# Kernel optimization log

Measured on AMD Instinct MI355X. Metric: run time of the kernel, lower is better.

Reference implementation:

```python
import jax, jax.numpy as jnp
import numpy as np

HEIGHT = 10
IN_DIM = 256
OUT_DIM = 16
BATCH = 65536


def _and_weight(height):
    # Fixed +/-1 tree-structured routing matrix [leaf_nodes, int_nodes]
    int_nodes = 2 ** height - 1
    leaf = 2 ** height
    w = np.zeros((leaf, int_nodes), dtype=np.float32)
    for i in range(height):
        num = 2 ** i
        start = num - 1
        for j in range(start, start + num):
            rb = leaf // num * (j - start)
            rm = rb + leaf // (2 * num)
            re = rb + leaf // num
            w[rb:rm, j] = 1.0
            w[rm:re, j] = -1.0
    return jnp.asarray(w)


def setup_inputs() -> dict:
    key = jax.random.key(0)
    k0, k1, k2, k3 = jax.random.split(key, 4)
    int_nodes = 2 ** HEIGHT - 1
    leaf = 2 ** HEIGHT
    return {
        "x": jax.random.normal(k0, (BATCH, IN_DIM), jnp.float32),
        "W_pred": jax.random.normal(k1, (int_nodes, IN_DIM), jnp.float32) / np.float32(np.sqrt(IN_DIM)),
        "b_pred": jnp.zeros((int_nodes,), jnp.float32),
        "W_or": jax.random.normal(k2, (OUT_DIM, leaf), jnp.float32) / np.float32(np.sqrt(leaf)),
        "action_stds": jax.random.normal(k3, (OUT_DIM, leaf), jnp.float32),
    }


def reference(x, W_pred, b_pred, W_or, action_stds):
    # predicate linear: [B, int_nodes]
    pred_z = x @ W_pred.T + b_pred
    # ScaleBinarizer1 (STE): scale = mean |z| per sample, binarize to {0, fac}
    fac = jax.lax.stop_gradient(jnp.mean(jnp.abs(pred_z), axis=-1, keepdims=True))
    hard = jnp.where(pred_z >= 0, fac, jnp.zeros_like(fac))
    pred_bin = pred_z + jax.lax.stop_gradient(hard - pred_z)  # straight-through
    pred_a = 2.0 * pred_bin - fac  # +/- fac (sign of pred_z scaled)
    # fixed tree AND layer: [B, leaf]
    W_and = _and_weight(HEIGHT)
    and_z = pred_a @ W_and.T
    and_a = jax.nn.softmax(and_z, axis=-1)
    # Sparser1 (STE): hard one-hot of the argmax leaf
    onehot = jax.nn.one_hot(jnp.argmax(and_a, axis=-1), and_a.shape[-1], dtype=and_a.dtype)
    and_a = and_a + jax.lax.stop_gradient(onehot - and_a)
    # OR layer + softmax over classes
    or_z = and_a @ W_or.T  # [B, out_dim]
    out = jax.nn.softmax(or_z, axis=-1)
    # per-action std: sum over leaves of and_a * action_stds, clamped
    std = jnp.clip(jnp.einsum("bl,ol->bo", and_a, action_stds), -20.0, 2.0)
    return out, std
```

## Files before the change

kernel.cpp:

```cpp
#include <hip/hip_runtime.h>
#include <stdint.h>


#define BATCH   65536
#define IN_DIM  256
#define NLEVEL  10
#define NLEAF   1024
#define OUT_DIM 16
#define EPS_TIE 0.02f
#define WB_U32  (1023 * 128)

#define DPP_QUAD_XOR1   0xB1
#define DPP_QUAD_XOR2   0x4E
#define DPP_HALF_MIRROR 0x141

template <int CTRL>
__device__ __forceinline__ float dpp_xfer(float v) {
    return __int_as_float(__builtin_amdgcn_update_dpp(
        0, __float_as_int(v), CTRL, 0xf, 0xf, true));
}
__device__ __forceinline__ float group8_sum(float v) {
    v += dpp_xfer<DPP_QUAD_XOR1>(v);
    v += dpp_xfer<DPP_QUAD_XOR2>(v);
    v += dpp_xfer<DPP_HALF_MIRROR>(v);
    return v;
}
__device__ __forceinline__ float group8_max(float v) {
    v = fmaxf(v, dpp_xfer<DPP_QUAD_XOR1>(v));
    v = fmaxf(v, dpp_xfer<DPP_QUAD_XOR2>(v));
    v = fmaxf(v, dpp_xfer<DPP_HALF_MIRROR>(v));
    return v;
}

__device__ __forceinline__ float blo(uint32_t u) { return __uint_as_float(u << 16); }
__device__ __forceinline__ float bhi(uint32_t u) { return __uint_as_float(u & 0xffff0000u); }

__global__ __launch_bounds__(256) void dgt_prep(
    const float* __restrict__ W, uint32_t* __restrict__ Wb)
{
    int i = blockIdx.x * 256 + threadIdx.x;
    if (i < WB_U32) {
        uint32_t ua = __float_as_uint(W[2 * i]);
        uint32_t ub = __float_as_uint(W[2 * i + 1]);
        uint32_t ra = (ua + 0x7fffu + ((ua >> 16) & 1u)) >> 16;
        uint32_t rb = (ub + 0x7fffu + ((ub >> 16) & 1u)) >> 16;
        Wb[i] = ra | (rb << 16);
    }
}

__device__ __forceinline__ int tree_sign_f64(
    float4 x0a, float4 x0b, float4 x1a, float4 x1b,
    float4 x2a, float4 x2b, float4 x3a, float4 x3b,
    const float* wrow, float bias, int l)
{
    double A0 = 0.0, A1 = 0.0, A2 = 0.0, A3 = 0.0;
#define ACC64(K, XA, XB)                                                     \
    {                                                                        \
        float4 wa = *reinterpret_cast<const float4*>(wrow + (K)*64 + l * 8); \
        float4 wb = *reinterpret_cast<const float4*>(wrow + (K)*64 + l * 8 + 4); \
        A0 += (double)XA.x * (double)wa.x; A1 += (double)XA.y * (double)wa.y; \
        A2 += (double)XA.z * (double)wa.z; A3 += (double)XA.w * (double)wa.w; \
        A0 += (double)XB.x * (double)wb.x; A1 += (double)XB.y * (double)wb.y; \
        A2 += (double)XB.z * (double)wb.z; A3 += (double)XB.w * (double)wb.w; \
    }
    ACC64(0, x0a, x0b) ACC64(1, x1a, x1b) ACC64(2, x2a, x2b) ACC64(3, x3a, x3b)
#undef ACC64
    double Z = (A0 + A1) + (A2 + A3);
    #pragma unroll
    for (int off = 4; off > 0; off >>= 1)
        Z += __shfl_xor(Z, off, 64);
    Z += (double)bias;
    return (Z < 0.0) ? 1 : 0;
}

__global__ __launch_bounds__(256, 2) void dgt_bf16(
    const float* __restrict__ x,
    const uint32_t* __restrict__ Wb,
    const float* __restrict__ W_pred,
    const float* __restrict__ b_pred,
    const float* __restrict__ W_or,
    const float* __restrict__ a_std,
    float* __restrict__ out)
{
    const int lane = threadIdx.x & 63;
    const int wid  = threadIdx.x >> 6;
    const int l    = lane & 7;
    const int g    = lane >> 3;
    const int sample = blockIdx.x * 32 + wid * 8 + g;

    const float* xrow = x + (size_t)sample * IN_DIM;
    float4 x0a = *reinterpret_cast<const float4*>(xrow +   0 + l * 8);
    float4 x0b = *reinterpret_cast<const float4*>(xrow +   4 + l * 8);
    float4 x1a = *reinterpret_cast<const float4*>(xrow +  64 + l * 8);
    float4 x1b = *reinterpret_cast<const float4*>(xrow +  68 + l * 8);
    float4 x2a = *reinterpret_cast<const float4*>(xrow + 128 + l * 8);
    float4 x2b = *reinterpret_cast<const float4*>(xrow + 132 + l * 8);
    float4 x3a = *reinterpret_cast<const float4*>(xrow + 192 + l * 8);
    float4 x3b = *reinterpret_cast<const float4*>(xrow + 196 + l * 8);

    int node = 0, pos = 0;
    float bcur = b_pred[0];

    #pragma unroll
    for (int lvl = 0; lvl < NLEVEL; ++lvl) {
        const uint32_t* wb = Wb + (size_t)node * 128;
        uint4 u0 = *reinterpret_cast<const uint4*>(wb +  0 + l * 4);
        uint4 u1 = *reinterpret_cast<const uint4*>(wb + 32 + l * 4);
        uint4 u2 = *reinterpret_cast<const uint4*>(wb + 64 + l * 4);
        uint4 u3 = *reinterpret_cast<const uint4*>(wb + 96 + l * 4);

        float bL = 0.f, bR = 0.f;
        if (lvl < NLEVEL - 1) {
            bL = b_pred[2 * node + 1];
            bR = b_pred[2 * node + 2];
        }

        float a0 = 0.f, a1 = 0.f, a2 = 0.f, a3 = 0.f;
#define ACCB(U, XA, XB)                                     \
        a0 += XA.x * blo(U.x); a1 += XA.y * bhi(U.x);       \
        a2 += XA.z * blo(U.y); a3 += XA.w * bhi(U.y);       \
        a0 += XB.x * blo(U.z); a1 += XB.y * bhi(U.z);       \
        a2 += XB.z * blo(U.w); a3 += XB.w * bhi(U.w);
        ACCB(u0, x0a, x0b)
        ACCB(u1, x1a, x1b)
        ACCB(u2, x2a, x2b)
        ACCB(u3, x3a, x3b)
#undef ACCB
        float z = group8_sum((a0 + a1) + (a2 + a3)) + bcur;

        int right;
        if (__builtin_expect(fabsf(z) >= EPS_TIE, 1))
            right = (z < 0.f) ? 1 : 0;
        else
            right = tree_sign_f64(x0a, x0b, x1a, x1b, x2a, x2b, x3a, x3b,
                                  W_pred + (size_t)node * IN_DIM, bcur, l);

        pos  = 2 * pos + right;
        node = 2 * node + 1 + right;
        if (lvl < NLEVEL - 1) bcur = right ? bR : bL;
    }
    const int leaf = pos;

    float zx = W_or[(size_t)(2 * l)     * NLEAF + leaf];
    float zy = W_or[(size_t)(2 * l + 1) * NLEAF + leaf];
    float m  = group8_max(fmaxf(zx, zy));
    float ex = __expf(zx - m), ey = __expf(zy - m);
    float s  = group8_sum(ex + ey);
    *reinterpret_cast<float2*>(out + (size_t)sample * OUT_DIM + 2 * l) =
        make_float2(ex / s, ey / s);

    float dx = a_std[(size_t)(2 * l)     * NLEAF + leaf];
    float dy = a_std[(size_t)(2 * l + 1) * NLEAF + leaf];
    *reinterpret_cast<float2*>(out + (size_t)BATCH * OUT_DIM
                               + (size_t)sample * OUT_DIM + 2 * l) =
        make_float2(fminf(fmaxf(dx, -20.f), 2.f),
                    fminf(fmaxf(dy, -20.f), 2.f));
}

__device__ __forceinline__ int tree_sign_f64_r8(
    float4 x0, float4 x1, float4 x2, float4 x3,
    float4 x4, float4 x5, float4 x6, float4 x7,
    const float* wrow, float bias, int l)
{
    double A0 = 0.0, A1 = 0.0, A2 = 0.0, A3 = 0.0;
#define ACC64(K, XV)                                                        \
    {                                                                       \
        float4 w = *reinterpret_cast<const float4*>(wrow + (K)*32 + l * 4); \
        A0 += (double)XV.x * (double)w.x; A1 += (double)XV.y * (double)w.y; \
        A2 += (double)XV.z * (double)w.z; A3 += (double)XV.w * (double)w.w; \
    }
    ACC64(0, x0) ACC64(1, x1) ACC64(2, x2) ACC64(3, x3)
    ACC64(4, x4) ACC64(5, x5) ACC64(6, x6) ACC64(7, x7)
#undef ACC64
    double Z = (A0 + A1) + (A2 + A3);
    #pragma unroll
    for (int off = 4; off > 0; off >>= 1)
        Z += __shfl_xor(Z, off, 64);
    Z += (double)bias;
    return (Z < 0.0) ? 1 : 0;
}

__global__ __launch_bounds__(256, 2) void dgt_f32(
    const float* __restrict__ x,
    const float* __restrict__ W_pred,
    const float* __restrict__ b_pred,
    const float* __restrict__ W_or,
    const float* __restrict__ a_std,
    float* __restrict__ out)
{
    const int lane = threadIdx.x & 63;
    const int wid  = threadIdx.x >> 6;
    const int l    = lane & 7;
    const int g    = lane >> 3;
    const int sample = blockIdx.x * 32 + wid * 8 + g;

    const float* xrow = x + (size_t)sample * IN_DIM;
    float4 x0 = *reinterpret_cast<const float4*>(xrow +   0 + l * 4);
    float4 x1 = *reinterpret_cast<const float4*>(xrow +  32 + l * 4);
    float4 x2 = *reinterpret_cast<const float4*>(xrow +  64 + l * 4);
    float4 x3 = *reinterpret_cast<const float4*>(xrow +  96 + l * 4);
    float4 x4 = *reinterpret_cast<const float4*>(xrow + 128 + l * 4);
    float4 x5 = *reinterpret_cast<const float4*>(xrow + 160 + l * 4);
    float4 x6 = *reinterpret_cast<const float4*>(xrow + 192 + l * 4);
    float4 x7 = *reinterpret_cast<const float4*>(xrow + 224 + l * 4);

    int node = 0, pos = 0;
    float bcur = b_pred[0];
    const float* wrow = W_pred;

    #pragma unroll
    for (int lvl = 0; lvl < NLEVEL; ++lvl) {
        float4 w0 = *reinterpret_cast<const float4*>(wrow +   0 + l * 4);
        float4 w1 = *reinterpret_cast<const float4*>(wrow +  32 + l * 4);
        float4 w2 = *reinterpret_cast<const float4*>(wrow +  64 + l * 4);
        float4 w3 = *reinterpret_cast<const float4*>(wrow +  96 + l * 4);
        float4 w4 = *reinterpret_cast<const float4*>(wrow + 128 + l * 4);
        float4 w5 = *reinterpret_cast<const float4*>(wrow + 160 + l * 4);
        float4 w6 = *reinterpret_cast<const float4*>(wrow + 192 + l * 4);
        float4 w7 = *reinterpret_cast<const float4*>(wrow + 224 + l * 4);

        float bL = 0.f, bR = 0.f;
        if (lvl < NLEVEL - 1) {
            bL = b_pred[2 * node + 1];
            bR = b_pred[2 * node + 2];
        }

        float a0, a1, a2, a3;
        a0  = x0.x * w0.x; a1  = x0.y * w0.y; a2  = x0.z * w0.z; a3  = x0.w * w0.w;
        a0 += x1.x * w1.x; a1 += x1.y * w1.y; a2 += x1.z * w1.z; a3 += x1.w * w1.w;
        a0 += x2.x * w2.x; a1 += x2.y * w2.y; a2 += x2.z * w2.z; a3 += x2.w * w2.w;
        a0 += x3.x * w3.x; a1 += x3.y * w3.y; a2 += x3.z * w3.z; a3 += x3.w * w3.w;
        a0 += x4.x * w4.x; a1 += x4.y * w4.y; a2 += x4.z * w4.z; a3 += x4.w * w4.w;
        a0 += x5.x * w5.x; a1 += x5.y * w5.y; a2 += x5.z * w5.z; a3 += x5.w * w5.w;
        a0 += x6.x * w6.x; a1 += x6.y * w6.y; a2 += x6.z * w6.z; a3 += x6.w * w6.w;
        a0 += x7.x * w7.x; a1 += x7.y * w7.y; a2 += x7.z * w7.z; a3 += x7.w * w7.w;
        float z = group8_sum((a0 + a1) + (a2 + a3)) + bcur;

        int right;
        if (__builtin_expect(fabsf(z) >= 1e-3f, 1))
            right = (z < 0.f) ? 1 : 0;
        else
            right = tree_sign_f64_r8(x0, x1, x2, x3, x4, x5, x6, x7,
                                     wrow, bcur, l);

        pos  = 2 * pos + right;
        node = 2 * node + 1 + right;
        if (lvl < NLEVEL - 1) {
            bcur = right ? bR : bL;
            wrow = W_pred + (size_t)node * IN_DIM;
        }
    }
    const int leaf = pos;

    float zx = W_or[(size_t)(2 * l)     * NLEAF + leaf];
    float zy = W_or[(size_t)(2 * l + 1) * NLEAF + leaf];
    float m  = group8_max(fmaxf(zx, zy));
    float ex = __expf(zx - m), ey = __expf(zy - m);
    float s  = group8_sum(ex + ey);
    *reinterpret_cast<float2*>(out + (size_t)sample * OUT_DIM + 2 * l) =
        make_float2(ex / s, ey / s);

    float dx = a_std[(size_t)(2 * l)     * NLEAF + leaf];
    float dy = a_std[(size_t)(2 * l + 1) * NLEAF + leaf];
    *reinterpret_cast<float2*>(out + (size_t)BATCH * OUT_DIM
                               + (size_t)sample * OUT_DIM + 2 * l) =
        make_float2(fminf(fmaxf(dx, -20.f), 2.f),
                    fminf(fmaxf(dy, -20.f), 2.f));
}

extern "C" void kernel_launch(void* const* d_in, const int* in_sizes, int n_in,
                              void* d_out, int out_size, void* d_ws, size_t ws_size,
                              hipStream_t stream) {
    const float* x      = (const float*)d_in[0];
    const float* W_pred = (const float*)d_in[1];
    const float* b_pred = (const float*)d_in[2];
    const float* W_or   = (const float*)d_in[3];
    const float* a_std  = (const float*)d_in[4];
    float* out = (float*)d_out;

    if (ws_size >= (size_t)WB_U32 * 4) {
        uint32_t* Wb = (uint32_t*)d_ws;
        hipLaunchKernelGGL(dgt_prep, dim3((WB_U32 + 255) / 256), dim3(256),
                           0, stream, W_pred, Wb);
        hipLaunchKernelGGL(dgt_bf16, dim3(BATCH / 32), dim3(256), 0, stream,
                           x, Wb, W_pred, b_pred, W_or, a_std, out);
    } else {
        hipLaunchKernelGGL(dgt_f32, dim3(BATCH / 32), dim3(256), 0, stream,
                           x, W_pred, b_pred, W_or, a_std, out);
    }
}
```

Baseline: 43.09 us.

## Stage top tree levels' bf16 weights in LDS, use fp32 global for last two levels

Each block of 512 threads copies the bf16-packed weights for the first 255 internal nodes (levels 0-7) into padded LDS and walks those levels from shared memory. The last two levels read full fp32 rows from global memory with a tighter tie threshold, so the bf16 conversion now covers only the staged rows. Blocks double in size to amortise the roughly 130 KB LDS fill. The fill is a large per-block cost, and the LDS footprint probably limits occupancy to one block per CU.

```diff
diff --git a/kernel.cpp b/kernel.cpp
--- a/kernel.cpp
+++ b/kernel.cpp
@@ -2,13 +2,14 @@
 #include <stdint.h>
 
 
-#define BATCH   65536
-#define IN_DIM  256
-#define NLEVEL  10
-#define NLEAF   1024
-#define OUT_DIM 16
-#define EPS_TIE 0.02f
-#define WB_U32  (1023 * 128)
+#define BATCH     65536
+#define IN_DIM    256
+#define NLEAF     1024
+#define OUT_DIM   16
+#define LDS_ROWS  255
+#define ROW_U32   128
+#define ROW_PAD   132
+#define STAGE_U32 (LDS_ROWS * ROW_U32)
 
 #define DPP_QUAD_XOR1   0xB1
 #define DPP_QUAD_XOR2   0x4E
@@ -39,7 +40,7 @@
     const float* __restrict__ W, uint32_t* __restrict__ Wb)
 {
     int i = blockIdx.x * 256 + threadIdx.x;
-    if (i < WB_U32) {
+    if (i < STAGE_U32) {
         uint32_t ua = __float_as_uint(W[2 * i]);
         uint32_t ub = __float_as_uint(W[2 * i + 1]);
         uint32_t ra = (ua + 0x7fffu + ((ua >> 16) & 1u)) >> 16;
@@ -73,7 +74,7 @@
     return (Z < 0.0) ? 1 : 0;
 }
 
-__global__ __launch_bounds__(256, 2) void dgt_bf16(
+__global__ __launch_bounds__(512, 2) void dgt_main(
     const float* __restrict__ x,
     const uint32_t* __restrict__ Wb,
     const float* __restrict__ W_pred,
@@ -82,11 +83,29 @@
     const float* __restrict__ a_std,
     float* __restrict__ out)
 {
+    __shared__ __align__(16) uint32_t sW[LDS_ROWS * ROW_PAD];
+
+    {
+        const uint4* src = reinterpret_cast<const uint4*>(Wb);
+        #pragma unroll
+        for (int s = 0; s < 16; ++s) {
+            int q = threadIdx.x + s * 512;
+            if (q < STAGE_U32 / 4) {
+                int j   = q * 4;
+                int row = j >> 7;
+                int col = j & 127;
+                uint4 v = src[q];
+                *reinterpret_cast<uint4*>(&sW[row * ROW_PAD + col]) = v;
+            }
+        }
+    }
+    __syncthreads();
+
     const int lane = threadIdx.x & 63;
     const int wid  = threadIdx.x >> 6;
     const int l    = lane & 7;
     const int g    = lane >> 3;
-    const int sample = blockIdx.x * 32 + wid * 8 + g;
+    const int sample = blockIdx.x * 64 + wid * 8 + g;
 
     const float* xrow = x + (size_t)sample * IN_DIM;
     float4 x0a = *reinterpret_cast<const float4*>(xrow +   0 + l * 8);
@@ -102,18 +121,15 @@
     float bcur = b_pred[0];
 
     #pragma unroll
-    for (int lvl = 0; lvl < NLEVEL; ++lvl) {
-        const uint32_t* wb = Wb + (size_t)node * 128;
-        uint4 u0 = *reinterpret_cast<const uint4*>(wb +  0 + l * 4);
-        uint4 u1 = *reinterpret_cast<const uint4*>(wb + 32 + l * 4);
-        uint4 u2 = *reinterpret_cast<const uint4*>(wb + 64 + l * 4);
-        uint4 u3 = *reinterpret_cast<const uint4*>(wb + 96 + l * 4);
-
-        float bL = 0.f, bR = 0.f;
-        if (lvl < NLEVEL - 1) {
-            bL = b_pred[2 * node + 1];
-            bR = b_pred[2 * node + 2];
-        }
+    for (int lvl = 0; lvl < 8; ++lvl) {
+        const uint32_t* wr = sW + node * ROW_PAD;
+        uint4 u0 = *reinterpret_cast<const uint4*>(wr +  0 + l * 4);
+        uint4 u1 = *reinterpret_cast<const uint4*>(wr + 32 + l * 4);
+        uint4 u2 = *reinterpret_cast<const uint4*>(wr + 64 + l * 4);
+        uint4 u3 = *reinterpret_cast<const uint4*>(wr + 96 + l * 4);
+
+        float bL = b_pred[2 * node + 1];
+        float bR = b_pred[2 * node + 2];
 
         float a0 = 0.f, a1 = 0.f, a2 = 0.f, a3 = 0.f;
 #define ACCB(U, XA, XB)                                     \
@@ -129,7 +145,7 @@
         float z = group8_sum((a0 + a1) + (a2 + a3)) + bcur;
 
         int right;
-        if (__builtin_expect(fabsf(z) >= EPS_TIE, 1))
+        if (__builtin_expect(fabsf(z) >= 0.02f, 1))
             right = (z < 0.f) ? 1 : 0;
         else
             right = tree_sign_f64(x0a, x0b, x1a, x1b, x2a, x2b, x3a, x3b,
@@ -137,7 +153,48 @@
 
         pos  = 2 * pos + right;
         node = 2 * node + 1 + right;
-        if (lvl < NLEVEL - 1) bcur = right ? bR : bL;
+        bcur = right ? bR : bL;
+    }
+
+    #pragma unroll
+    for (int lvl = 8; lvl < 10; ++lvl) {
+        const float* wrow = W_pred + (size_t)node * IN_DIM;
+        float4 w0a = *reinterpret_cast<const float4*>(wrow +   0 + l * 8);
+        float4 w0b = *reinterpret_cast<const float4*>(wrow +   4 + l * 8);
+        float4 w1a = *reinterpret_cast<const float4*>(wrow +  64 + l * 8);
+        float4 w1b = *reinterpret_cast<const float4*>(wrow +  68 + l * 8);
+        float4 w2a = *reinterpret_cast<const float4*>(wrow + 128 + l * 8);
+        float4 w2b = *reinterpret_cast<const float4*>(wrow + 132 + l * 8);
+        float4 w3a = *reinterpret_cast<const float4*>(wrow + 192 + l * 8);
+        float4 w3b = *reinterpret_cast<const float4*>(wrow + 196 + l * 8);
+
+        float bL = 0.f, bR = 0.f;
+        if (lvl < 9) {
+            bL = b_pred[2 * node + 1];
+            bR = b_pred[2 * node + 2];
+        }
+
+        float a0, a1, a2, a3;
+        a0  = x0a.x * w0a.x; a1  = x0a.y * w0a.y; a2  = x0a.z * w0a.z; a3  = x0a.w * w0a.w;
+        a0 += x0b.x * w0b.x; a1 += x0b.y * w0b.y; a2 += x0b.z * w0b.z; a3 += x0b.w * w0b.w;
+        a0 += x1a.x * w1a.x; a1 += x1a.y * w1a.y; a2 += x1a.z * w1a.z; a3 += x1a.w * w1a.w;
+        a0 += x1b.x * w1b.x; a1 += x1b.y * w1b.y; a2 += x1b.z * w1b.z; a3 += x1b.w * w1b.w;
+        a0 += x2a.x * w2a.x; a1 += x2a.y * w2a.y; a2 += x2a.z * w2a.z; a3 += x2a.w * w2a.w;
+        a0 += x2b.x * w2b.x; a1 += x2b.y * w2b.y; a2 += x2b.z * w2b.z; a3 += x2b.w * w2b.w;
+        a0 += x3a.x * w3a.x; a1 += x3a.y * w3a.y; a2 += x3a.z * w3a.z; a3 += x3a.w * w3a.w;
+        a0 += x3b.x * w3b.x; a1 += x3b.y * w3b.y; a2 += x3b.z * w3b.z; a3 += x3b.w * w3b.w;
+        float z = group8_sum((a0 + a1) + (a2 + a3)) + bcur;
+
+        int right;
+        if (__builtin_expect(fabsf(z) >= 1e-3f, 1))
+            right = (z < 0.f) ? 1 : 0;
+        else
+            right = tree_sign_f64(x0a, x0b, x1a, x1b, x2a, x2b, x3a, x3b,
+                                  wrow, bcur, l);
+
+        pos  = 2 * pos + right;
+        node = 2 * node + 1 + right;
+        if (lvl < 9) bcur = right ? bR : bL;
     }
     const int leaf = pos;
 
@@ -209,7 +266,7 @@
     const float* wrow = W_pred;
 
     #pragma unroll
-    for (int lvl = 0; lvl < NLEVEL; ++lvl) {
+    for (int lvl = 0; lvl < 10; ++lvl) {
         float4 w0 = *reinterpret_cast<const float4*>(wrow +   0 + l * 4);
         float4 w1 = *reinterpret_cast<const float4*>(wrow +  32 + l * 4);
         float4 w2 = *reinterpret_cast<const float4*>(wrow +  64 + l * 4);
@@ -220,7 +277,7 @@
         float4 w7 = *reinterpret_cast<const float4*>(wrow + 224 + l * 4);
 
         float bL = 0.f, bR = 0.f;
-        if (lvl < NLEVEL - 1) {
+        if (lvl < 9) {
             bL = b_pred[2 * node + 1];
             bR = b_pred[2 * node + 2];
         }
@@ -245,7 +302,7 @@
 
         pos  = 2 * pos + right;
         node = 2 * node + 1 + right;
-        if (lvl < NLEVEL - 1) {
+        if (lvl < 9) {
             bcur = right ? bR : bL;
             wrow = W_pred + (size_t)node * IN_DIM;
         }
@@ -278,11 +335,11 @@
     const float* a_std  = (const float*)d_in[4];
     float* out = (float*)d_out;
 
-    if (ws_size >= (size_t)WB_U32 * 4) {
+    if (ws_size >= (size_t)STAGE_U32 * 4) {
         uint32_t* Wb = (uint32_t*)d_ws;
-        hipLaunchKernelGGL(dgt_prep, dim3((WB_U32 + 255) / 256), dim3(256),
+        hipLaunchKernelGGL(dgt_prep, dim3((STAGE_U32 + 255) / 256), dim3(256),
                            0, stream, W_pred, Wb);
-        hipLaunchKernelGGL(dgt_bf16, dim3(BATCH / 32), dim3(256), 0, stream,
+        hipLaunchKernelGGL(dgt_main, dim3(BATCH / 64), dim3(512), 0, stream,
                            x, Wb, W_pred, b_pred, W_or, a_std, out);
     } else {
         hipLaunchKernelGGL(dgt_f32, dim3(BATCH / 32), dim3(256), 0, stream,
```

New measurement: 46.37 us. +7.6%, slower.

## Pack x rows to bf16 registers and raise occupancy in tree traversal kernel

Applied to the files above, without the earlier changes.

The main kernel now keeps each sample's x slice as 16 packed bf16 registers instead of 32 fp32 registers. Launch bounds rise from 2 to 5 blocks per SM, and the fp64 tie-break path reloads x from global memory rather than holding it live. Weight loads are split into two halves around a scheduling barrier, and the bias is loaded per level instead of prefetching both children. The aim is more waves in flight to hide the latency of the dependent per-level gathers, at the cost of extra bf16 rounding of x, which could flip near-tie decisions outside the epsilon band, and a serial bias load on each level's critical path.

```diff
diff --git a/kernel.cpp b/kernel.cpp
--- a/kernel.cpp
+++ b/kernel.cpp
@@ -35,36 +35,36 @@
 __device__ __forceinline__ float blo(uint32_t u) { return __uint_as_float(u << 16); }
 __device__ __forceinline__ float bhi(uint32_t u) { return __uint_as_float(u & 0xffff0000u); }
 
+__device__ __forceinline__ uint32_t pkbf(float a, float b) {
+    uint32_t ua = __float_as_uint(a), ub = __float_as_uint(b);
+    uint32_t ra = (ua + 0x7fffu + ((ua >> 16) & 1u)) >> 16;
+    uint32_t rb = (ub + 0x7fffu + ((ub >> 16) & 1u)) >> 16;
+    return ra | (rb << 16);
+}
+
 __global__ __launch_bounds__(256) void dgt_prep(
     const float* __restrict__ W, uint32_t* __restrict__ Wb)
 {
     int i = blockIdx.x * 256 + threadIdx.x;
-    if (i < WB_U32) {
-        uint32_t ua = __float_as_uint(W[2 * i]);
-        uint32_t ub = __float_as_uint(W[2 * i + 1]);
-        uint32_t ra = (ua + 0x7fffu + ((ua >> 16) & 1u)) >> 16;
-        uint32_t rb = (ub + 0x7fffu + ((ub >> 16) & 1u)) >> 16;
-        Wb[i] = ra | (rb << 16);
-    }
+    if (i < WB_U32) Wb[i] = pkbf(W[2 * i], W[2 * i + 1]);
 }
 
 __device__ __forceinline__ int tree_sign_f64(
-    float4 x0a, float4 x0b, float4 x1a, float4 x1b,
-    float4 x2a, float4 x2b, float4 x3a, float4 x3b,
-    const float* wrow, float bias, int l)
+    const float* __restrict__ xrow, const float* __restrict__ wrow,
+    float bias, int l)
 {
     double A0 = 0.0, A1 = 0.0, A2 = 0.0, A3 = 0.0;
-#define ACC64(K, XA, XB)                                                     \
-    {                                                                        \
-        float4 wa = *reinterpret_cast<const float4*>(wrow + (K)*64 + l * 8); \
-        float4 wb = *reinterpret_cast<const float4*>(wrow + (K)*64 + l * 8 + 4); \
-        A0 += (double)XA.x * (double)wa.x; A1 += (double)XA.y * (double)wa.y; \
-        A2 += (double)XA.z * (double)wa.z; A3 += (double)XA.w * (double)wa.w; \
-        A0 += (double)XB.x * (double)wb.x; A1 += (double)XB.y * (double)wb.y; \
-        A2 += (double)XB.z * (double)wb.z; A3 += (double)XB.w * (double)wb.w; \
-    }
-    ACC64(0, x0a, x0b) ACC64(1, x1a, x1b) ACC64(2, x2a, x2b) ACC64(3, x3a, x3b)
-#undef ACC64
+    #pragma unroll
+    for (int k = 0; k < 4; ++k) {
+        float4 xa = *reinterpret_cast<const float4*>(xrow + k * 64 + l * 8);
+        float4 xb = *reinterpret_cast<const float4*>(xrow + k * 64 + l * 8 + 4);
+        float4 wa = *reinterpret_cast<const float4*>(wrow + k * 64 + l * 8);
+        float4 wb = *reinterpret_cast<const float4*>(wrow + k * 64 + l * 8 + 4);
+        A0 += (double)xa.x * (double)wa.x; A1 += (double)xa.y * (double)wa.y;
+        A2 += (double)xa.z * (double)wa.z; A3 += (double)xa.w * (double)wa.w;
+        A0 += (double)xb.x * (double)wb.x; A1 += (double)xb.y * (double)wb.y;
+        A2 += (double)xb.z * (double)wb.z; A3 += (double)xb.w * (double)wb.w;
+    }
     double Z = (A0 + A1) + (A2 + A3);
     #pragma unroll
     for (int off = 4; off > 0; off >>= 1)
@@ -73,7 +73,7 @@
     return (Z < 0.0) ? 1 : 0;
 }
 
-__global__ __launch_bounds__(256, 2) void dgt_bf16(
+__global__ __launch_bounds__(256, 5) void dgt_b16(
     const float* __restrict__ x,
     const uint32_t* __restrict__ Wb,
     const float* __restrict__ W_pred,
@@ -89,55 +89,64 @@
     const int sample = blockIdx.x * 32 + wid * 8 + g;
 
     const float* xrow = x + (size_t)sample * IN_DIM;
-    float4 x0a = *reinterpret_cast<const float4*>(xrow +   0 + l * 8);
-    float4 x0b = *reinterpret_cast<const float4*>(xrow +   4 + l * 8);
-    float4 x1a = *reinterpret_cast<const float4*>(xrow +  64 + l * 8);
-    float4 x1b = *reinterpret_cast<const float4*>(xrow +  68 + l * 8);
-    float4 x2a = *reinterpret_cast<const float4*>(xrow + 128 + l * 8);
-    float4 x2b = *reinterpret_cast<const float4*>(xrow + 132 + l * 8);
-    float4 x3a = *reinterpret_cast<const float4*>(xrow + 192 + l * 8);
-    float4 x3b = *reinterpret_cast<const float4*>(xrow + 196 + l * 8);
+    uint32_t p0, p1, p2, p3, p4, p5, p6, p7, p8, p9, p10, p11, p12, p13, p14, p15;
+    {
+        float4 a0 = *reinterpret_cast<const float4*>(xrow +   0 + l * 8);
+        float4 b0 = *reinterpret_cast<const float4*>(xrow +   4 + l * 8);
+        float4 a1 = *reinterpret_cast<const float4*>(xrow +  64 + l * 8);
+        float4 b1 = *reinterpret_cast<const float4*>(xrow +  68 + l * 8);
+        p0 = pkbf(a0.x, a0.y); p1 = pkbf(a0.z, a0.w);
+        p2 = pkbf(b0.x, b0.y); p3 = pkbf(b0.z, b0.w);
+        p4 = pkbf(a1.x, a1.y); p5 = pkbf(a1.z, a1.w);
+        p6 = pkbf(b1.x, b1.y); p7 = pkbf(b1.z, b1.w);
+        float4 a2 = *reinterpret_cast<const float4*>(xrow + 128 + l * 8);
+        float4 b2 = *reinterpret_cast<const float4*>(xrow + 132 + l * 8);
+        float4 a3 = *reinterpret_cast<const float4*>(xrow + 192 + l * 8);
+        float4 b3 = *reinterpret_cast<const float4*>(xrow + 196 + l * 8);
+        p8  = pkbf(a2.x, a2.y); p9  = pkbf(a2.z, a2.w);
+        p10 = pkbf(b2.x, b2.y); p11 = pkbf(b2.z, b2.w);
+        p12 = pkbf(a3.x, a3.y); p13 = pkbf(a3.z, a3.w);
+        p14 = pkbf(b3.x, b3.y); p15 = pkbf(b3.z, b3.w);
+    }
 
     int node = 0, pos = 0;
-    float bcur = b_pred[0];
 
     #pragma unroll
     for (int lvl = 0; lvl < NLEVEL; ++lvl) {
         const uint32_t* wb = Wb + (size_t)node * 128;
-        uint4 u0 = *reinterpret_cast<const uint4*>(wb +  0 + l * 4);
-        uint4 u1 = *reinterpret_cast<const uint4*>(wb + 32 + l * 4);
-        uint4 u2 = *reinterpret_cast<const uint4*>(wb + 64 + l * 4);
-        uint4 u3 = *reinterpret_cast<const uint4*>(wb + 96 + l * 4);
-
-        float bL = 0.f, bR = 0.f;
-        if (lvl < NLEVEL - 1) {
-            bL = b_pred[2 * node + 1];
-            bR = b_pred[2 * node + 2];
-        }
+        float bcur = b_pred[node];
+
+        uint4 A0 = *reinterpret_cast<const uint4*>(wb +  0 + l * 4);
+        uint4 A1 = *reinterpret_cast<const uint4*>(wb + 32 + l * 4);
 
         float a0 = 0.f, a1 = 0.f, a2 = 0.f, a3 = 0.f;
-#define ACCB(U, XA, XB)                                     \
-        a0 += XA.x * blo(U.x); a1 += XA.y * bhi(U.x);       \
-        a2 += XA.z * blo(U.y); a3 += XA.w * bhi(U.y);       \
-        a0 += XB.x * blo(U.z); a1 += XB.y * bhi(U.z);       \
-        a2 += XB.z * blo(U.w); a3 += XB.w * bhi(U.w);
-        ACCB(u0, x0a, x0b)
-        ACCB(u1, x1a, x1b)
-        ACCB(u2, x2a, x2b)
-        ACCB(u3, x3a, x3b)
-#undef ACCB
+#define FMAU(U, P)                                          \
+        a0 += blo(U) * blo(P); a1 += bhi(U) * bhi(P);
+#define FMA4(UQ, Pa, Pb, Pc, Pd)                            \
+        FMAU(UQ.x, Pa) FMAU(UQ.y, Pb) FMAU(UQ.z, Pc) FMAU(UQ.w, Pd)
+        FMA4(A0, p0, p1, p2, p3)
+        FMA4(A1, p4, p5, p6, p7)
+
+        __builtin_amdgcn_sched_barrier(0);
+
+        uint4 B0 = *reinterpret_cast<const uint4*>(wb + 64 + l * 4);
+        uint4 B1 = *reinterpret_cast<const uint4*>(wb + 96 + l * 4);
+        FMA4(B0, p8,  p9,  p10, p11)
+        FMA4(B1, p12, p13, p14, p15)
+#undef FMA4
+#undef FMAU
+
         float z = group8_sum((a0 + a1) + (a2 + a3)) + bcur;
 
         int right;
         if (__builtin_expect(fabsf(z) >= EPS_TIE, 1))
             right = (z < 0.f) ? 1 : 0;
         else
-            right = tree_sign_f64(x0a, x0b, x1a, x1b, x2a, x2b, x3a, x3b,
-                                  W_pred + (size_t)node * IN_DIM, bcur, l);
+            right = tree_sign_f64(xrow, W_pred + (size_t)node * IN_DIM,
+                                  bcur, l);
 
         pos  = 2 * pos + right;
         node = 2 * node + 1 + right;
-        if (lvl < NLEVEL - 1) bcur = right ? bR : bL;
     }
     const int leaf = pos;
 
@@ -282,7 +291,7 @@
         uint32_t* Wb = (uint32_t*)d_ws;
         hipLaunchKernelGGL(dgt_prep, dim3((WB_U32 + 255) / 256), dim3(256),
                            0, stream, W_pred, Wb);
-        hipLaunchKernelGGL(dgt_bf16, dim3(BATCH / 32), dim3(256), 0, stream,
+        hipLaunchKernelGGL(dgt_b16, dim3(BATCH / 32), dim3(256), 0, stream,
                            x, Wb, W_pred, b_pred, W_or, a_std, out);
     } else {
         hipLaunchKernelGGL(dgt_f32, dim3(BATCH / 32), dim3(256), 0, stream,
```

After: 45.86 us. +6.4%, slower.
